# Kernel optimization log

Hardware: AMD Instinct MI355X
Metric: run time of the kernel (lower is better)

The kernel has to match this reference:

```python
import jax, jax.numpy as jnp
import numpy as np

N_CONS = 10000
N_COLS = 10000
N = N_CONS + N_COLS
E = 200000
NEG_SLOPE = 0.2  # PyG GATConv default negative_slope


def gat_conv(x, edge_index, W, att_src, att_dst, bias, heads, out_ch):
    """PyG-style GATConv (eval mode, add_self_loops=True, concat=True)."""
    n = x.shape[0]
    loops = jnp.arange(n, dtype=edge_index.dtype)
    ei = jnp.concatenate([edge_index, jnp.stack([loops, loops])], axis=1)
    src, dst = ei[0], ei[1]                      # message flows src -> dst
    xp = (x @ W.T).reshape(n, heads, out_ch)     # [N, H, C]
    a_src = jnp.einsum('nhc,hc->nh', xp, att_src)  # [N, H]
    a_dst = jnp.einsum('nhc,hc->nh', xp, att_dst)
    e = jax.nn.leaky_relu(a_src[src] + a_dst[dst], NEG_SLOPE)  # [E', H]
    # segment softmax over edges sharing a destination node
    m = jax.ops.segment_max(e, dst, num_segments=n)
    p = jnp.exp(e - m[dst])
    denom = jax.ops.segment_sum(p, dst, num_segments=n)
    alpha = p / (denom[dst] + 1e-16)
    out = jax.ops.segment_sum(alpha[:, :, None] * xp[src], dst, num_segments=n)
    return out.reshape(n, heads * out_ch) + bias


def setup_inputs() -> dict:
    key = jax.random.key(0)
    ks = jax.random.split(key, 16)
    s = 0.05
    return {
        'constraints_state': jax.random.normal(ks[0], (N_CONS, 4), jnp.float32),
        'columns_state': jax.random.normal(ks[1], (N_COLS, 8), jnp.float32),
        'node_W': jax.random.normal(ks[2], (128, 8), jnp.float32) * s,
        'node_b': jnp.zeros((128,), jnp.float32),
        'col_W': jax.random.normal(ks[3], (128, 16), jnp.float32) * s,
        'col_b': jnp.zeros((128,), jnp.float32),
        'W1': jax.random.normal(ks[4], (1024, 128), jnp.float32) * s,
        'att_src1': jax.random.normal(ks[5], (8, 128), jnp.float32) * s,
        'att_dst1': jax.random.normal(ks[6], (8, 128), jnp.float32) * s,
        'b1': jnp.zeros((1024,), jnp.float32),
        'W2': jax.random.normal(ks[7], (128, 1024), jnp.float32) * s,
        'att_src2': jax.random.normal(ks[8], (1, 128), jnp.float32) * s,
        'att_dst2': jax.random.normal(ks[9], (1, 128), jnp.float32) * s,
        'b2': jnp.zeros((128,), jnp.float32),
        'out_W': jax.random.normal(ks[10], (128, 128), jnp.float32) * s,
        'out_b': jnp.zeros((128,), jnp.float32),
        'edges': jax.random.randint(ks[11], (2, E), 0, N, dtype=jnp.int64),
    }


def reference(constraints_state, columns_state, node_W, node_b, col_W, col_b,
              W1, att_src1, att_dst1, b1, W2, att_src2, att_dst2, b2,
              out_W, out_b, edges):
    # feature_gain=2: repeat features along the feature axis
    nf = jnp.tile(constraints_state, (1, 2))   # [N_CONS, 8]
    cf = jnp.tile(columns_state, (1, 2))       # [N_COLS, 16]
    ne = jax.nn.relu(nf @ node_W.T + node_b)
    ce = jax.nn.relu(cf @ col_W.T + col_b)
    emb = jnp.concatenate([ne, ce], axis=0)    # [N, 128]
    emb = jax.nn.relu(gat_conv(emb, edges, W1, att_src1, att_dst1, b1, 8, 128))
    # torch.flip(edges, [1]) on [2,E] reverses edge ordering (same semantics)
    emb = jax.nn.relu(gat_conv(emb, jnp.flip(edges, axis=1), W2,
                               att_src2, att_dst2, b2, 1, 128))
    logits = emb[-N_COLS:] @ out_W.T + out_b   # [N_COLS, 128]
    return logits
```

## Files before the change

### kernel.cpp

```cpp
#include <hip/hip_runtime.h>

#define NCONS 10000
#define NCOLSN 10000
#define NNODES 20000
#define NEDGE 200000
#define NETOT 220000
#define NEG_SLOPE 0.2f
#define NSCANB 79

typedef unsigned short u16;
typedef __attribute__((ext_vector_type(8))) short bf16x8;
typedef __attribute__((ext_vector_type(4))) float f32x4;

__device__ __forceinline__ float bf2f(u16 u) {
  return __uint_as_float(((unsigned int)u) << 16);
}
__device__ __forceinline__ u16 f2bf(float f) {
  unsigned int x = __float_as_uint(f);
  return (u16)((x + 0x7fffu + ((x >> 16) & 1u)) >> 16);
}
__device__ __forceinline__ float lrelu(float v) {
  return v >= 0.f ? v : NEG_SLOPE * v;
}
__device__ __forceinline__ void gl2lds16(const u16* g, u16* l) {
  __builtin_amdgcn_global_load_lds(
      (const __attribute__((address_space(1))) unsigned int*)g,
      (__attribute__((address_space(3))) unsigned int*)l, 16, 0, 0);
}
__device__ __forceinline__ float readlane_f(float v, int j) {
  return __uint_as_float(__builtin_amdgcn_readlane(__float_as_uint(v), j));
}

#define W1N (1024 * 128)
#define W2N (128 * 1024)
#define OWN (128 * 128)
#define EMB0N (NNODES * 128)
#define WSDN (16 * 128)

__global__ void prep(const float* __restrict__ cons, const float* __restrict__ cols,
                     const float* __restrict__ nW, const float* __restrict__ nb,
                     const float* __restrict__ cW, const float* __restrict__ cb,
                     const float* __restrict__ W1, const float* __restrict__ W2,
                     const float* __restrict__ oW, const float* __restrict__ att_s1,
                     const float* __restrict__ att_d1, u16* __restrict__ emb,
                     u16* __restrict__ Wbf, u16* __restrict__ wsd,
                     const int* __restrict__ edges, int* __restrict__ counts) {
  int idx = blockIdx.x * 256 + threadIdx.x;
  if (idx < NETOT) {
    int dst = (idx < NEDGE) ? edges[NEDGE + idx] : (idx - NEDGE);
    atomicAdd(&counts[dst], 1);
  }
  if (idx < EMB0N) {
    int row = idx >> 7, o = idx & 127;
    float acc;
    if (row < NCONS) {
      acc = nb[o];
      #pragma unroll
      for (int k = 0; k < 4; ++k)
        acc += cons[row * 4 + k] * (nW[o * 8 + k] + nW[o * 8 + 4 + k]);
    } else {
      int r = row - NCONS;
      acc = cb[o];
      #pragma unroll
      for (int k = 0; k < 8; ++k)
        acc += cols[r * 8 + k] * (cW[o * 16 + k] + cW[o * 16 + 8 + k]);
    }
    emb[idx] = f2bf(fmaxf(acc, 0.f));
    return;
  }
  int i = idx - EMB0N;
  if (i < W1N + W2N + OWN) {
    float v;
    if (i < W1N) v = W1[i];
    else if (i < W1N + W2N) v = W2[i - W1N];
    else v = oW[i - W1N - W2N];
    Wbf[i] = f2bf(v);
    return;
  }
  int i2 = i - (W1N + W2N + OWN);
  if (i2 < WSDN) {
    int vec = i2 >> 7, k = i2 & 127;
    int h = vec & 7;
    const float* att = (vec < 8) ? att_s1 : att_d1;
    float a = 0.f;
    #pragma unroll 8
    for (int c = 0; c < 128; ++c)
      a += att[h * 128 + c] * W1[(size_t)(h * 128 + c) * 128 + k];
    wsd[i2] = f2bf(a);
  }
}

__global__ void scan_a(const int* __restrict__ counts, int* __restrict__ lscan,
                       int* __restrict__ bsum) {
  __shared__ int sh[256];
  int t = threadIdx.x;
  int i = blockIdx.x * 256 + t;
  int v = (i < NNODES) ? counts[i] : 0;
  sh[t] = v;
  __syncthreads();
  for (int d = 1; d < 256; d <<= 1) {
    int add = (t >= d) ? sh[t - d] : 0;
    __syncthreads();
    sh[t] += add;
    __syncthreads();
  }
  lscan[i] = sh[t];
  if (t == 255) bsum[blockIdx.x] = sh[255];
}
__global__ void scan_c2(const int* __restrict__ lscan, const int* __restrict__ counts,
                        const int* __restrict__ bsum, int* __restrict__ offsets,
                        int* __restrict__ cursor) {
  __shared__ int sh[128];
  int t = threadIdx.x;
  if (t < 128) sh[t] = (t < NSCANB) ? bsum[t] : 0;
  __syncthreads();
  for (int d = 1; d < 128; d <<= 1) {
    int add = (t >= d && t < 128) ? sh[t - d] : 0;
    __syncthreads();
    if (t < 128) sh[t] += add;
    __syncthreads();
  }
  int bbase = (blockIdx.x > 0) ? sh[blockIdx.x - 1] : 0;
  int i = blockIdx.x * 256 + t;
  if (i == 0) offsets[0] = 0;
  if (i < NNODES) {
    int incl = lscan[i] + bbase;
    offsets[i + 1] = incl;
    cursor[i] = incl - counts[i];
  }
}

__global__ void fill_edges(const int* __restrict__ edges, int* __restrict__ cursor,
                           int* __restrict__ csr_src) {
  int i = blockIdx.x * 256 + threadIdx.x;
  if (i >= NETOT) return;
  int src, dst;
  if (i < NEDGE) { src = edges[i]; dst = edges[NEDGE + i]; }
  else { src = dst = i - NEDGE; }
  int pos = atomicAdd(&cursor[dst], 1);
  csr_src[pos] = src;
}

__global__ __launch_bounds__(256) void dots1_k(const u16* __restrict__ emb,
                                               const u16* __restrict__ wsd,
                                               float* __restrict__ as1,
                                               float* __restrict__ ad1) {
  int wv = threadIdx.x >> 6, lane = threadIdx.x & 63;
  int quad = lane >> 4, l16 = lane & 15;
  int m0 = blockIdx.x * 64 + wv * 16;
  int ra = m0 + l16; if (ra >= NNODES) ra = NNODES - 1;
  f32x4 acc = f32x4{0.f, 0.f, 0.f, 0.f};
  #pragma unroll
  for (int k0 = 0; k0 < 128; k0 += 32) {
    bf16x8 a = *(const bf16x8*)(emb + (size_t)ra * 128 + k0 + quad * 8);
    bf16x8 b = *(const bf16x8*)(wsd + (size_t)l16 * 128 + k0 + quad * 8);
    acc = __builtin_amdgcn_mfma_f32_16x16x32_bf16(a, b, acc, 0, 0, 0);
  }
  #pragma unroll
  for (int r = 0; r < 4; ++r) {
    int node = m0 + quad * 4 + r;
    if (node < NNODES) {
      if (l16 < 8) as1[node * 8 + l16] = acc[r];
      else         ad1[node * 8 + (l16 - 8)] = acc[r];
    }
  }
}

template <int BM, bool SLICED, bool DOTS, bool BIAS, bool RELU, bool OUTF32>
__global__ __launch_bounds__(256) void gemm_bt(const u16* __restrict__ A, const u16* __restrict__ B,
                                               const float* __restrict__ bias, void* __restrict__ Cv,
                                               const float* __restrict__ att_s,
                                               const float* __restrict__ att_d,
                                               float* __restrict__ a_srcO, float* __restrict__ a_dstO,
                                               int M, int N, int K, int lda, size_t aOff) {
  constexpr int MI = BM / 32;
  __shared__ u16 sA[BM * 32];
  __shared__ u16 sB[128 * 32];
  int tid = threadIdx.x;
  int wv = tid >> 6;
  int lane = tid & 63;
  int quad = lane >> 4;
  int l16 = lane & 15;
  int m0 = blockIdx.x * BM;
  int n0g = blockIdx.y * 128;
  int h = n0g >> 7;
  const u16* Ab = SLICED ? A + (size_t)h * aOff : A;
  const u16* Bb = SLICED ? B + (size_t)h * (size_t)128 * K : B;
  int brow0 = SLICED ? 0 : n0g;
  int rm = (wv >> 1) * (16 * MI);
  int cn = (wv & 1) * 64;

  f32x4 acc[MI][4];
  #pragma unroll
  for (int mi = 0; mi < MI; ++mi)
    #pragma unroll
    for (int ni = 0; ni < 4; ++ni) acc[mi][ni] = f32x4{0.f, 0.f, 0.f, 0.f};

  for (int k0 = 0; k0 < K; k0 += 32) {
    for (int off = tid * 16; off < BM * 64; off += 4096) {
      int row = off >> 6;
      int kk = (off & 63) >> 1;
      int rg = m0 + row; if (rg >= M) rg = M - 1;
      gl2lds16(Ab + (size_t)rg * lda + k0 + kk, &sA[off >> 1]);
    }
    for (int off = tid * 16; off < 128 * 64; off += 4096) {
      int row = off >> 6;
      int kk = (off & 63) >> 1;
      gl2lds16(Bb + (size_t)(brow0 + row) * K + k0 + kk, &sB[off >> 1]);
    }
    __syncthreads();
    bf16x8 af[MI], bf[4];
    #pragma unroll
    for (int mi = 0; mi < MI; ++mi)
      af[mi] = *(const bf16x8*)&sA[(rm + mi * 16 + l16) * 32 + quad * 8];
    #pragma unroll
    for (int ni = 0; ni < 4; ++ni)
      bf[ni] = *(const bf16x8*)&sB[(cn + ni * 16 + l16) * 32 + quad * 8];
    #pragma unroll
    for (int mi = 0; mi < MI; ++mi)
      #pragma unroll
      for (int ni = 0; ni < 4; ++ni)
        acc[mi][ni] = __builtin_amdgcn_mfma_f32_16x16x32_bf16(af[mi], bf[ni], acc[mi][ni], 0, 0, 0);
    __syncthreads();
  }

  if (DOTS) {
    float av_s[4], av_d[4];
    #pragma unroll
    for (int ni = 0; ni < 4; ++ni) {
      int col = n0g + cn + ni * 16 + l16;
      av_s[ni] = att_s[col];
      av_d[ni] = att_d[col];
    }
    int H = N >> 7;
    #pragma unroll
    for (int mi = 0; mi < MI; ++mi) {
      #pragma unroll
      for (int r = 0; r < 4; ++r) {
        float sp = 0.f, dp = 0.f;
        #pragma unroll
        for (int ni = 0; ni < 4; ++ni) {
          sp += acc[mi][ni][r] * av_s[ni];
          dp += acc[mi][ni][r] * av_d[ni];
        }
        #pragma unroll
        for (int w = 1; w < 16; w <<= 1) {
          sp += __shfl_xor(sp, w, 64);
          dp += __shfl_xor(dp, w, 64);
        }
        int orow = m0 + rm + mi * 16 + quad * 4 + r;
        if (l16 == 0 && orow < M) {
          atomicAdd(&a_srcO[(size_t)orow * H + h], sp);
          atomicAdd(&a_dstO[(size_t)orow * H + h], dp);
        }
      }
    }
  }
  #pragma unroll
  for (int ni = 0; ni < 4; ++ni) {
    int col = n0g + cn + ni * 16 + l16;
    float bv = BIAS ? bias[col] : 0.f;
    #pragma unroll
    for (int mi = 0; mi < MI; ++mi) {
      #pragma unroll
      for (int r = 0; r < 4; ++r) {
        int orow = m0 + rm + mi * 16 + quad * 4 + r;
        if (orow < M) {
          float v = acc[mi][ni][r] + bv;
          if (RELU) v = fmaxf(v, 0.f);
          if (OUTF32) ((float*)Cv)[(size_t)orow * N + col] = v;
          else        ((u16*)Cv)[(size_t)orow * N + col] = f2bf(v);
        }
      }
    }
  }
}

__global__ __launch_bounds__(256) void fagg1(const int* __restrict__ offs,
                                             const int* __restrict__ csr_src,
                                             const float* __restrict__ as1,
                                             const float* __restrict__ ad1,
                                             const u16* __restrict__ emb,
                                             u16* __restrict__ agg) {
  __shared__ float alds[4 * 512];
  int wvi = threadIdx.x >> 6;
  int dst = blockIdx.x * 4 + wvi;
  if (dst >= NNODES) return;
  int l = threadIdx.x & 63;
  int h = l & 7, i = l >> 3;
  float* wlds = &alds[wvi * 512];
  int off = offs[dst];
  int deg = offs[dst + 1] - off;
  const int* srcs = csr_src + off;
  float adv = ad1[dst * 8 + h];
  const u16* base = emb + l * 2;
  float acc[8][2];
  #pragma unroll
  for (int hh = 0; hh < 8; ++hh) { acc[hh][0] = 0.f; acc[hh][1] = 0.f; }

  if (deg <= 64) {
    int sl = srcs[l < deg ? l : deg - 1];
    float g[8];
    #pragma unroll
    for (int t = 0; t < 8; ++t) {
      int jj = t * 8 + i;
      int s = __builtin_amdgcn_readlane(sl, jj < deg ? jj : 0);
      g[t] = as1[s * 8 + h];
    }
    float m = -1e30f, ssum = 0.f, ev[8];
    #pragma unroll
    for (int t = 0; t < 8; ++t) {
      int jj = t * 8 + i;
      float e = (jj < deg) ? lrelu(g[t] + adv) : -1e30f;
      ev[t] = e;
      float nm = fmaxf(m, e);
      ssum = ssum * __expf(m - nm) + ((jj < deg) ? __expf(e - nm) : 0.f);
      m = nm;
    }
    #pragma unroll
    for (int w = 8; w < 64; w <<= 1) {
      float om = __shfl_xor(m, w, 64);
      float os = __shfl_xor(ssum, w, 64);
      float nm = fmaxf(m, om);
      ssum = ssum * __expf(m - nm) + os * __expf(om - nm);
      m = nm;
    }
    float inv = 1.f / (ssum + 1e-16f);
    #pragma unroll
    for (int t = 0; t < 8; ++t)
      wlds[t * 64 + l] = __expf(ev[t] - m) * inv;
    for (int j0 = 0; j0 < deg; j0 += 8) {
      ushort2 uu[8];
      #pragma unroll
      for (int t2 = 0; t2 < 8; ++t2) {
        int slot = j0 + t2;
        int s = __builtin_amdgcn_readlane(sl, slot < deg ? slot : 0);
        uu[t2] = *(const ushort2*)(base + (size_t)s * 128);
      }
      #pragma unroll
      for (int t2 = 0; t2 < 8; ++t2) {
        int slot = j0 + t2;
        float x0 = bf2f(uu[t2].x), x1 = bf2f(uu[t2].y);
        #pragma unroll
        for (int hh = 0; hh < 8; ++hh) {
          float w = wlds[slot * 8 + hh];
          acc[hh][0] += w * x0;
          acc[hh][1] += w * x1;
        }
      }
    }
  } else {
    float m = -1e30f, ssum = 0.f;
    for (int j = i; j < deg; j += 8) {
      int s = srcs[j];
      float e = lrelu(as1[s * 8 + h] + adv);
      float nm = fmaxf(m, e);
      ssum = ssum * __expf(m - nm) + __expf(e - nm);
      m = nm;
    }
    #pragma unroll
    for (int w = 8; w < 64; w <<= 1) {
      float om = __shfl_xor(m, w, 64);
      float os = __shfl_xor(ssum, w, 64);
      float nm = fmaxf(m, om);
      ssum = ssum * __expf(m - nm) + os * __expf(om - nm);
      m = nm;
    }
    float inv = 1.f / (ssum + 1e-16f);
    for (int b0 = 0; b0 < deg; b0 += 64) {
      int cnt = deg - b0; if (cnt > 64) cnt = 64;
      #pragma unroll
      for (int t = 0; t < 8; ++t) {
        int sl2 = t * 8 + i;
        float a = 0.f;
        if (sl2 < cnt) {
          int s = srcs[b0 + sl2];
          a = __expf(lrelu(as1[s * 8 + h] + adv) - m) * inv;
        }
        wlds[t * 64 + l] = a;
      }
      int sv = srcs[b0 + (l < cnt ? l : cnt - 1)];
      for (int j0 = 0; j0 < cnt; j0 += 8) {
        ushort2 uu[8];
        #pragma unroll
        for (int t2 = 0; t2 < 8; ++t2) {
          int slot = j0 + t2;
          int s = __builtin_amdgcn_readlane(sv, slot < cnt ? slot : 0);
          uu[t2] = *(const ushort2*)(base + (size_t)s * 128);
        }
        #pragma unroll
        for (int t2 = 0; t2 < 8; ++t2) {
          int slot = j0 + t2;
          float x0 = bf2f(uu[t2].x), x1 = bf2f(uu[t2].y);
          #pragma unroll
          for (int hh = 0; hh < 8; ++hh) {
            float w = wlds[slot * 8 + hh];
            acc[hh][0] += w * x0;
            acc[hh][1] += w * x1;
          }
        }
      }
    }
  }
  #pragma unroll
  for (int hh = 0; hh < 8; ++hh) {
    ushort2 o;
    o.x = f2bf(acc[hh][0]);
    o.y = f2bf(acc[hh][1]);
    *(ushort2*)(agg + (size_t)dst * 1024 + hh * 128 + l * 2) = o;
  }
}

__global__ __launch_bounds__(256) void fsp2(const int* __restrict__ offs,
                                            const int* __restrict__ csr_src,
                                            const float* __restrict__ a_src,
                                            const float* __restrict__ a_dst,
                                            const u16* __restrict__ xp2,
                                            const float* __restrict__ bias,
                                            u16* __restrict__ out) {
  int wvi = threadIdx.x >> 6;
  int dst = NCONS + blockIdx.x * 4 + wvi;
  if (dst >= NNODES) return;
  int l = threadIdx.x & 63;
  int off = offs[dst];
  int deg = offs[dst + 1] - off;
  const int* srcs = csr_src + off;
  float ad = a_dst[dst];
  const u16* base = xp2 + l * 2;
  float m = -1e30f, ssum = 0.f, a0 = 0.f, a1 = 0.f;
  for (int b0 = 0; b0 < deg; b0 += 64) {
    int cnt = deg - b0; if (cnt > 64) cnt = 64;
    int sv = srcs[b0 + (l < cnt ? l : cnt - 1)];
    float e = (l < cnt) ? lrelu(a_src[sv] + ad) : -1e30f;
    float mc = e;
    #pragma unroll
    for (int w = 1; w < 64; w <<= 1) mc = fmaxf(mc, __shfl_xor(mc, w, 64));
    float pex = __expf(e - mc);
    float sc = pex;
    #pragma unroll
    for (int w = 1; w < 64; w <<= 1) sc += __shfl_xor(sc, w, 64);
    float c0 = 0.f, c1 = 0.f;
    int j = 0;
    for (; j + 8 <= cnt; j += 8) {
      ushort2 uu[8];
      float ww[8];
      #pragma unroll
      for (int t = 0; t < 8; ++t) {
        int s = __builtin_amdgcn_readlane(sv, j + t);
        ww[t] = readlane_f(pex, j + t);
        uu[t] = *(const ushort2*)(base + (size_t)s * 128);
      }
      #pragma unroll
      for (int t = 0; t < 8; ++t) {
        c0 += ww[t] * bf2f(uu[t].x);
        c1 += ww[t] * bf2f(uu[t].y);
      }
    }
    for (; j < cnt; ++j) {
      int s = __builtin_amdgcn_readlane(sv, j);
      float w = readlane_f(pex, j);
      ushort2 u = *(const ushort2*)(base + (size_t)s * 128);
      c0 += w * bf2f(u.x);
      c1 += w * bf2f(u.y);
    }
    float nm = fmaxf(m, mc);
    float fo = __expf(m - nm), fn = __expf(mc - nm);
    a0 = a0 * fo + c0 * fn;
    a1 = a1 * fo + c1 * fn;
    ssum = ssum * fo + sc * fn;
    m = nm;
  }
  float inv = 1.f / (ssum + 1e-16f);
  int cg = l * 2;
  ushort2 o;
  o.x = f2bf(fmaxf(a0 * inv + bias[cg], 0.f));
  o.y = f2bf(fmaxf(a1 * inv + bias[cg + 1], 0.f));
  *(ushort2*)(out + (size_t)dst * 128 + cg) = o;
}

extern "C" void kernel_launch(void* const* d_in, const int* in_sizes, int n_in,
                              void* d_out, int out_size, void* d_ws, size_t ws_size,
                              hipStream_t stream) {
  const float* cons    = (const float*)d_in[0];
  const float* cols    = (const float*)d_in[1];
  const float* node_W  = (const float*)d_in[2];
  const float* node_b  = (const float*)d_in[3];
  const float* col_W   = (const float*)d_in[4];
  const float* col_b   = (const float*)d_in[5];
  const float* W1      = (const float*)d_in[6];
  const float* att_s1  = (const float*)d_in[7];
  const float* att_d1  = (const float*)d_in[8];
  const float* b1      = (const float*)d_in[9];
  const float* W2      = (const float*)d_in[10];
  const float* att_s2  = (const float*)d_in[11];
  const float* att_d2  = (const float*)d_in[12];
  const float* b2      = (const float*)d_in[13];
  const float* out_W   = (const float*)d_in[14];
  const float* out_b   = (const float*)d_in[15];
  const int* edges     = (const int*)d_in[16];

  char* p = (char*)d_ws;
  auto alloc = [&](size_t bytes) {
    char* r = p;
    p += (bytes + 255) & ~(size_t)255;
    return r;
  };
  u16* emb0    = (u16*)alloc((size_t)NNODES * 128 * 2);
  u16* agg     = (u16*)alloc((size_t)NNODES * 1024 * 2);
  u16* emb2    = (u16*)alloc((size_t)NNODES * 1024 * 2);
  u16* xp2     = (u16*)alloc((size_t)NNODES * 128 * 2);
  u16* emb3    = (u16*)alloc((size_t)NNODES * 128 * 2);
  u16* Wbf     = (u16*)alloc((size_t)(W1N + W2N + OWN) * 2);
  u16* wsd     = (u16*)alloc((size_t)WSDN * 2);
  float* as2   = (float*)alloc((size_t)NNODES * 4);
  float* ad2   = (float*)alloc((size_t)NNODES * 4);
  int* counts  = (int*)alloc((size_t)NNODES * 4);
  size_t zspan = (char*)(counts + NNODES) - (char*)as2;
  float* as1   = (float*)alloc((size_t)NNODES * 8 * 4);
  float* ad1   = (float*)alloc((size_t)NNODES * 8 * 4);
  int* offs    = (int*)alloc((size_t)(NNODES + 1) * 4);
  int* cursor  = (int*)alloc((size_t)NNODES * 4);
  int* csrsrc  = (int*)alloc((size_t)NETOT * 4);
  int* lscan   = (int*)alloc((size_t)NSCANB * 256 * 4);
  int* bsum    = (int*)alloc((size_t)NSCANB * 4);

  u16* W1bf = Wbf;
  u16* W2bf = Wbf + W1N;
  u16* oWbf = Wbf + W1N + W2N;

  hipMemsetAsync(as2, 0, zspan, stream);

  prep<<<(EMB0N + W1N + W2N + OWN + WSDN + 255) / 256, 256, 0, stream>>>(
      cons, cols, node_W, node_b, col_W, col_b, W1, W2, out_W, att_s1, att_d1,
      emb0, Wbf, wsd, edges, counts);

  scan_a<<<NSCANB, 256, 0, stream>>>(counts, lscan, bsum);
  scan_c2<<<NSCANB, 256, 0, stream>>>(lscan, counts, bsum, offs, cursor);
  fill_edges<<<(NETOT + 255) / 256, 256, 0, stream>>>(edges, cursor, csrsrc);

  dots1_k<<<(NNODES + 63) / 64, 256, 0, stream>>>(emb0, wsd, as1, ad1);
  fagg1<<<(NNODES + 3) / 4, 256, 0, stream>>>(offs, csrsrc, as1, ad1, emb0, agg);
  gemm_bt<128, true, false, true, true, false><<<dim3((NNODES + 127) / 128, 8), 256, 0, stream>>>(
      agg, W1bf, b1, emb2, nullptr, nullptr, nullptr, nullptr,
      NNODES, 1024, 128, 1024, 128);

  gemm_bt<32, false, true, false, false, false><<<dim3((NNODES + 31) / 32, 1), 256, 0, stream>>>(
      emb2, W2bf, nullptr, xp2, att_s2, att_d2, as2, ad2, NNODES, 128, 1024, 1024, 0);
  fsp2<<<(NCOLSN + 3) / 4, 256, 0, stream>>>(offs, csrsrc, as2, ad2, xp2, b2, emb3);

  gemm_bt<32, false, false, true, false, true><<<dim3((NCOLSN + 31) / 32, 1), 256, 0, stream>>>(
      emb3 + (size_t)NCONS * 128, oWbf, out_b, d_out, nullptr, nullptr, nullptr, nullptr,
      NCOLSN, 128, 128, 128, 0);
}
```

Before: 244.2 us.

## Fuse layer-1 output GEMM with layer-2 projection GEMM, keeping intermediate in LDS

The per-head W1 GEMM (with bias and ReLU) and the W2 projection GEMM with attention dots are merged into one kernel. Each block computes a 32-row slab of the 1024-wide layer-1 output into LDS, then multiplies it by W2, so the 20000x1024 bf16 intermediate never goes to global memory. The cost is a large LDS footprint (about 66KB per block), which lowers occupancy, and only 625 blocks that each do serial per-head work with small 32-row tiles and re-stream the W1/W2 weights per block. The generic gemm_bt template is trimmed to the one remaining use.

```diff
diff --git a/kernel.cpp b/kernel.cpp
--- a/kernel.cpp
+++ b/kernel.cpp
@@ -166,13 +166,118 @@
   }
 }
 
-template <int BM, bool SLICED, bool DOTS, bool BIAS, bool RELU, bool OUTF32>
+__global__ __launch_bounds__(256) void gemm12(const u16* __restrict__ agg,
+                                              const u16* __restrict__ W1bf,
+                                              const float* __restrict__ b1,
+                                              const u16* __restrict__ W2bf,
+                                              const float* __restrict__ att_s,
+                                              const float* __restrict__ att_d,
+                                              float* __restrict__ as2,
+                                              float* __restrict__ ad2,
+                                              u16* __restrict__ xp2) {
+  __shared__ u16 E[32 * 1028];
+  __shared__ u16 sA[32 * 32];
+  __shared__ u16 sB[128 * 32];
+  int tid = threadIdx.x;
+  int wv = tid >> 6, lane = tid & 63, quad = lane >> 4, l16 = lane & 15;
+  int m0 = blockIdx.x * 32;
+  int rm = (wv >> 1) * 16, cn = (wv & 1) * 64;
+
+  for (int h = 0; h < 8; ++h) {
+    f32x4 acc[4];
+    #pragma unroll
+    for (int ni = 0; ni < 4; ++ni) acc[ni] = f32x4{0.f, 0.f, 0.f, 0.f};
+    for (int k0 = 0; k0 < 128; k0 += 32) {
+      if (tid < 128) {
+        int off = tid * 16;
+        int row = off >> 6, kk = (off & 63) >> 1;
+        gl2lds16(agg + (size_t)(m0 + row) * 1024 + h * 128 + k0 + kk, &sA[off >> 1]);
+      }
+      for (int off = tid * 16; off < 128 * 64; off += 4096) {
+        int row = off >> 6, kk = (off & 63) >> 1;
+        gl2lds16(W1bf + (size_t)(h * 128 + row) * 128 + k0 + kk, &sB[off >> 1]);
+      }
+      __syncthreads();
+      bf16x8 af = *(const bf16x8*)&sA[(rm + l16) * 32 + quad * 8];
+      #pragma unroll
+      for (int ni = 0; ni < 4; ++ni) {
+        bf16x8 bfv = *(const bf16x8*)&sB[(cn + ni * 16 + l16) * 32 + quad * 8];
+        acc[ni] = __builtin_amdgcn_mfma_f32_16x16x32_bf16(af, bfv, acc[ni], 0, 0, 0);
+      }
+      __syncthreads();
+    }
+    #pragma unroll
+    for (int ni = 0; ni < 4; ++ni) {
+      int col = cn + ni * 16 + l16;
+      float bv = b1[h * 128 + col];
+      #pragma unroll
+      for (int r = 0; r < 4; ++r) {
+        int row = rm + quad * 4 + r;
+        E[row * 1028 + h * 128 + col] = f2bf(fmaxf(acc[ni][r] + bv, 0.f));
+      }
+    }
+    __syncthreads();
+  }
+
+  f32x4 acc2[4];
+  #pragma unroll
+  for (int ni = 0; ni < 4; ++ni) acc2[ni] = f32x4{0.f, 0.f, 0.f, 0.f};
+  for (int k0 = 0; k0 < 1024; k0 += 32) {
+    for (int off = tid * 16; off < 128 * 64; off += 4096) {
+      int row = off >> 6, kk = (off & 63) >> 1;
+      gl2lds16(W2bf + (size_t)row * 1024 + k0 + kk, &sB[off >> 1]);
+    }
+    __syncthreads();
+    bf16x8 af = *(const bf16x8*)&E[(rm + l16) * 1028 + k0 + quad * 8];
+    #pragma unroll
+    for (int ni = 0; ni < 4; ++ni) {
+      bf16x8 bfv = *(const bf16x8*)&sB[(cn + ni * 16 + l16) * 32 + quad * 8];
+      acc2[ni] = __builtin_amdgcn_mfma_f32_16x16x32_bf16(af, bfv, acc2[ni], 0, 0, 0);
+    }
+    __syncthreads();
+  }
+
+  float av_s[4], av_d[4];
+  #pragma unroll
+  for (int ni = 0; ni < 4; ++ni) {
+    int col = cn + ni * 16 + l16;
+    av_s[ni] = att_s[col];
+    av_d[ni] = att_d[col];
+  }
+  #pragma unroll
+  for (int r = 0; r < 4; ++r) {
+    float sp = 0.f, dp = 0.f;
+    #pragma unroll
+    for (int ni = 0; ni < 4; ++ni) {
+      sp += acc2[ni][r] * av_s[ni];
+      dp += acc2[ni][r] * av_d[ni];
+    }
+    #pragma unroll
+    for (int w = 1; w < 16; w <<= 1) {
+      sp += __shfl_xor(sp, w, 64);
+      dp += __shfl_xor(dp, w, 64);
+    }
+    int orow = m0 + rm + quad * 4 + r;
+    if (l16 == 0) {
+      atomicAdd(&as2[orow], sp);
+      atomicAdd(&ad2[orow], dp);
+    }
+  }
+  #pragma unroll
+  for (int ni = 0; ni < 4; ++ni) {
+    int col = cn + ni * 16 + l16;
+    #pragma unroll
+    for (int r = 0; r < 4; ++r) {
+      int orow = m0 + rm + quad * 4 + r;
+      xp2[(size_t)orow * 128 + col] = f2bf(acc2[ni][r]);
+    }
+  }
+}
+
+template <int BM>
 __global__ __launch_bounds__(256) void gemm_bt(const u16* __restrict__ A, const u16* __restrict__ B,
-                                               const float* __restrict__ bias, void* __restrict__ Cv,
-                                               const float* __restrict__ att_s,
-                                               const float* __restrict__ att_d,
-                                               float* __restrict__ a_srcO, float* __restrict__ a_dstO,
-                                               int M, int N, int K, int lda, size_t aOff) {
+                                               const float* __restrict__ bias, float* __restrict__ C,
+                                               int M, int N, int K) {
   constexpr int MI = BM / 32;
   __shared__ u16 sA[BM * 32];
   __shared__ u16 sB[128 * 32];
@@ -182,11 +287,6 @@
   int quad = lane >> 4;
   int l16 = lane & 15;
   int m0 = blockIdx.x * BM;
-  int n0g = blockIdx.y * 128;
-  int h = n0g >> 7;
-  const u16* Ab = SLICED ? A + (size_t)h * aOff : A;
-  const u16* Bb = SLICED ? B + (size_t)h * (size_t)128 * K : B;
-  int brow0 = SLICED ? 0 : n0g;
   int rm = (wv >> 1) * (16 * MI);
   int cn = (wv & 1) * 64;
 
@@ -201,76 +301,39 @@
       int row = off >> 6;
       int kk = (off & 63) >> 1;
       int rg = m0 + row; if (rg >= M) rg = M - 1;
-      gl2lds16(Ab + (size_t)rg * lda + k0 + kk, &sA[off >> 1]);
+      gl2lds16(A + (size_t)rg * K + k0 + kk, &sA[off >> 1]);
     }
     for (int off = tid * 16; off < 128 * 64; off += 4096) {
       int row = off >> 6;
       int kk = (off & 63) >> 1;
-      gl2lds16(Bb + (size_t)(brow0 + row) * K + k0 + kk, &sB[off >> 1]);
-    }
-    __syncthreads();
-    bf16x8 af[MI], bf[4];
+      gl2lds16(B + (size_t)row * K + k0 + kk, &sB[off >> 1]);
+    }
+    __syncthreads();
+    bf16x8 af[MI], bfv[4];
     #pragma unroll
     for (int mi = 0; mi < MI; ++mi)
       af[mi] = *(const bf16x8*)&sA[(rm + mi * 16 + l16) * 32 + quad * 8];
     #pragma unroll
     for (int ni = 0; ni < 4; ++ni)
-      bf[ni] = *(const bf16x8*)&sB[(cn + ni * 16 + l16) * 32 + quad * 8];
+      bfv[ni] = *(const bf16x8*)&sB[(cn + ni * 16 + l16) * 32 + quad * 8];
     #pragma unroll
     for (int mi = 0; mi < MI; ++mi)
       #pragma unroll
       for (int ni = 0; ni < 4; ++ni)
-        acc[mi][ni] = __builtin_amdgcn_mfma_f32_16x16x32_bf16(af[mi], bf[ni], acc[mi][ni], 0, 0, 0);
-    __syncthreads();
-  }
-
-  if (DOTS) {
-    float av_s[4], av_d[4];
-    #pragma unroll
-    for (int ni = 0; ni < 4; ++ni) {
-      int col = n0g + cn + ni * 16 + l16;
-      av_s[ni] = att_s[col];
-      av_d[ni] = att_d[col];
-    }
-    int H = N >> 7;
-    #pragma unroll
-    for (int mi = 0; mi < MI; ++mi) {
-      #pragma unroll
-      for (int r = 0; r < 4; ++r) {
-        float sp = 0.f, dp = 0.f;
-        #pragma unroll
-        for (int ni = 0; ni < 4; ++ni) {
-          sp += acc[mi][ni][r] * av_s[ni];
-          dp += acc[mi][ni][r] * av_d[ni];
-        }
-        #pragma unroll
-        for (int w = 1; w < 16; w <<= 1) {
-          sp += __shfl_xor(sp, w, 64);
-          dp += __shfl_xor(dp, w, 64);
-        }
-        int orow = m0 + rm + mi * 16 + quad * 4 + r;
-        if (l16 == 0 && orow < M) {
-          atomicAdd(&a_srcO[(size_t)orow * H + h], sp);
-          atomicAdd(&a_dstO[(size_t)orow * H + h], dp);
-        }
-      }
-    }
-  }
+        acc[mi][ni] = __builtin_amdgcn_mfma_f32_16x16x32_bf16(af[mi], bfv[ni], acc[mi][ni], 0, 0, 0);
+    __syncthreads();
+  }
+
   #pragma unroll
   for (int ni = 0; ni < 4; ++ni) {
-    int col = n0g + cn + ni * 16 + l16;
-    float bv = BIAS ? bias[col] : 0.f;
+    int col = cn + ni * 16 + l16;
+    float bv = bias[col];
     #pragma unroll
     for (int mi = 0; mi < MI; ++mi) {
       #pragma unroll
       for (int r = 0; r < 4; ++r) {
         int orow = m0 + rm + mi * 16 + quad * 4 + r;
-        if (orow < M) {
-          float v = acc[mi][ni][r] + bv;
-          if (RELU) v = fmaxf(v, 0.f);
-          if (OUTF32) ((float*)Cv)[(size_t)orow * N + col] = v;
-          else        ((u16*)Cv)[(size_t)orow * N + col] = f2bf(v);
-        }
+        if (orow < M) C[(size_t)orow * N + col] = acc[mi][ni][r] + bv;
       }
     }
   }
@@ -507,7 +570,6 @@
   };
   u16* emb0    = (u16*)alloc((size_t)NNODES * 128 * 2);
   u16* agg     = (u16*)alloc((size_t)NNODES * 1024 * 2);
-  u16* emb2    = (u16*)alloc((size_t)NNODES * 1024 * 2);
   u16* xp2     = (u16*)alloc((size_t)NNODES * 128 * 2);
   u16* emb3    = (u16*)alloc((size_t)NNODES * 128 * 2);
   u16* Wbf     = (u16*)alloc((size_t)(W1N + W2N + OWN) * 2);
@@ -540,15 +602,12 @@
 
   dots1_k<<<(NNODES + 63) / 64, 256, 0, stream>>>(emb0, wsd, as1, ad1);
   fagg1<<<(NNODES + 3) / 4, 256, 0, stream>>>(offs, csrsrc, as1, ad1, emb0, agg);
-  gemm_bt<128, true, false, true, true, false><<<dim3((NNODES + 127) / 128, 8), 256, 0, stream>>>(
-      agg, W1bf, b1, emb2, nullptr, nullptr, nullptr, nullptr,
-      NNODES, 1024, 128, 1024, 128);
-
-  gemm_bt<32, false, true, false, false, false><<<dim3((NNODES + 31) / 32, 1), 256, 0, stream>>>(
-      emb2, W2bf, nullptr, xp2, att_s2, att_d2, as2, ad2, NNODES, 128, 1024, 1024, 0);
+
+  gemm12<<<NNODES / 32, 256, 0, stream>>>(agg, W1bf, b1, W2bf, att_s2, att_d2,
+                                          as2, ad2, xp2);
+
   fsp2<<<(NCOLSN + 3) / 4, 256, 0, stream>>>(offs, csrsrc, as2, ad2, xp2, b2, emb3);
 
-  gemm_bt<32, false, false, true, false, true><<<dim3((NCOLSN + 31) / 32, 1), 256, 0, stream>>>(
-      emb3 + (size_t)NCONS * 128, oWbf, out_b, d_out, nullptr, nullptr, nullptr, nullptr,
-      NCOLSN, 128, 128, 128, 0);
-}
+  gemm_bt<32><<<(NCOLSN + 31) / 32, 256, 0, stream>>>(
+      emb3 + (size_t)NCONS * 128, oWbf, out_b, (float*)d_out, NCOLSN, 128, 128);
+}
```

Measured after the change: 252.6 us. 3.4% more time.
